# Performance work log

Hardware: AMD Instinct MI355X
Metric: run time of the kernel (lower is better)

Reference implementation:

```python
import jax, jax.numpy as jnp
from jax import lax
import numpy as np

KSIZE = 21

def setup_inputs() -> dict:
    key = jax.random.key(0)
    k1, k2 = jax.random.split(key)
    x = jax.random.normal(k1, (32, 3, 512, 512), dtype=jnp.float32)
    kernel = jax.random.uniform(k2, (32, 1, KSIZE, KSIZE), dtype=jnp.float32)
    return {"x": x, "kernel": kernel}

def reference(x, kernel):
    # Per-sample depthwise conv: fuse batch loop into a single grouped conv
    # by folding batch into channels (groups = B*C).
    B, C, H, W = x.shape
    K = kernel.shape[-1]
    pad = K // 2
    # expand the per-sample kernel across channels, shape (B*C, 1, K, K)
    k = jnp.broadcast_to(kernel, (B, C, K, K)).reshape(B * C, 1, K, K)
    xr = x.reshape(1, B * C, H, W)
    out = lax.conv_general_dilated(
        xr, k,
        window_strides=(1, 1),
        padding=[(pad, pad), (pad, pad)],
        dimension_numbers=("NCHW", "OIHW", "NCHW"),
        feature_group_count=B * C,
    )
    return out.reshape(B, C, H, W)
```

## Files before the change

### kernel.cpp

```cpp
#include <hip/hip_runtime.h>

#define KK 21
#define HH 512
#define WW 512
#define CC 3
#define BB 32
#define TILE_Y 64
#define TILE_X 128
#define SROWS 84
#define SSTRIDE 168
#define NB_PER_B 21504
#define NCHUNK 41

typedef __attribute__((ext_vector_type(8))) short short8;
typedef __attribute__((ext_vector_type(4))) float floatx4;

__device__ __forceinline__ unsigned short f2bf(float f) {
    union { float f; unsigned u; } v; v.f = f;
    unsigned r = v.u + 0x7FFF + ((v.u >> 16) & 1);
    return (unsigned short)(r >> 16);
}

__global__ __launch_bounds__(256) void build_B(
    const float* __restrict__ ker, unsigned short* __restrict__ wsB)
{
    const int b = blockIdx.x;
    const float* __restrict__ kp = ker + b * KK * KK;
    unsigned short* __restrict__ wb = wsB + (size_t)b * NB_PER_B;
    for (int e = threadIdx.x; e < NB_PER_B; e += 256) {
        const int j  = e & 7;
        const int n  = (e >> 3) & 15;
        const int q  = (e >> 7) & 3;
        const int h  = (e >> 9) & 1;
        const int kh = e >> 10;
        const int d  = q * 8 + j - n;
        float v = 0.0f;
        if (h == 0) { if (d >= 0 && d < 16) v = kp[kh * KK + d]; }
        else        { if (d >= 0 && d < 5)  v = kp[kh * KK + 16 + d]; }
        wb[e] = f2bf(v);
    }
}

__global__ __launch_bounds__(256, 5) void dwconv_mfma(
    const float* __restrict__ x,
    const unsigned short* __restrict__ wsB,
    float* __restrict__ out)
{
    __shared__ __align__(16) unsigned short s_in[SROWS * SSTRIDE];

    const int tiles = (HH / TILE_Y) * (WW / TILE_X);
    const int bc = blockIdx.x / tiles;
    const int t  = blockIdx.x % tiles;
    const int ty0 = (t / (WW / TILE_X)) * TILE_Y;
    const int tx0 = (t % (WW / TILE_X)) * TILE_X;
    const int b = bc / CC;

    const float* __restrict__ xp = x + (size_t)bc * HH * WW;
    const unsigned short* __restrict__ wsb = wsB + (size_t)b * NB_PER_B;
    const int tid = threadIdx.x;

    for (int i = tid; i < SROWS * NCHUNK; i += 256) {
        const int ly = i / NCHUNK;
        const int k  = i - ly * NCHUNK;
        const int gy = ty0 - 10 + ly;
        const int gx0 = tx0 - 12 + 4 * k;
        const int lc0 = 4 * k - 2;
        float4 v = make_float4(0.f, 0.f, 0.f, 0.f);
        if (gy >= 0 && gy < HH) {
            const float* __restrict__ rp = xp + (size_t)gy * WW;
            if (gx0 >= 0 && gx0 + 3 < WW) {
                v = *(const float4*)(rp + gx0);
            } else {
                if (gx0 + 0 >= 0 && gx0 + 0 < WW) v.x = rp[gx0 + 0];
                if (gx0 + 1 >= 0 && gx0 + 1 < WW) v.y = rp[gx0 + 1];
                if (gx0 + 2 >= 0 && gx0 + 2 < WW) v.z = rp[gx0 + 2];
                if (gx0 + 3 >= 0 && gx0 + 3 < WW) v.w = rp[gx0 + 3];
            }
        }
        const unsigned p0 = (unsigned)f2bf(v.x) | ((unsigned)f2bf(v.y) << 16);
        const unsigned p1 = (unsigned)f2bf(v.z) | ((unsigned)f2bf(v.w) << 16);
        unsigned* row = (unsigned*)&s_in[ly * SSTRIDE];
        if (lc0 >= 0) row[lc0 >> 1] = p0;
        row[(lc0 >> 1) + 1] = p1;
    }
    __syncthreads();

    const int lane = tid & 63;
    const int wv   = tid >> 6;
    const int mrow = lane & 15;
    const int qd   = lane >> 4;

    floatx4 acc[8];
#pragma unroll
    for (int tt = 0; tt < 8; ++tt) acc[tt] = (floatx4){0.f, 0.f, 0.f, 0.f};

    const unsigned short* bbase = wsb + (qd * 16 + mrow) * 8;
    short8 nb1 = *(const short8*)(bbase);
    short8 nb2 = *(const short8*)(bbase + 512);

#pragma unroll 1
    for (int kh = 0; kh < KK; ++kh) {
        const short8 b1 = nb1;
        const short8 b2 = nb2;
        const int khn = (kh < KK - 1) ? (kh + 1) : kh;
        nb1 = *(const short8*)(bbase + khn * 1024);
        nb2 = *(const short8*)(bbase + khn * 1024 + 512);

        const unsigned short* arow = s_in + (16 * wv + kh + mrow) * SSTRIDE + 8 * qd;
        short8 a[9];
#pragma unroll
        for (int s = 0; s < 9; ++s) a[s] = *(const short8*)(arow + 16 * s);

#pragma unroll
        for (int tt = 0; tt < 8; ++tt) {
            acc[tt] = __builtin_amdgcn_mfma_f32_16x16x32_bf16(a[tt],     b1, acc[tt], 0, 0, 0);
            acc[tt] = __builtin_amdgcn_mfma_f32_16x16x32_bf16(a[tt + 1], b2, acc[tt], 0, 0, 0);
        }
    }

    float* __restrict__ op = out + (size_t)bc * HH * WW;
#pragma unroll
    for (int tt = 0; tt < 8; ++tt) {
#pragma unroll
        for (int r = 0; r < 4; ++r) {
            const int y = ty0 + 16 * wv + qd * 4 + r;
            const int xcol = tx0 + 16 * tt + mrow;
            op[(size_t)y * WW + xcol] = acc[tt][r];
        }
    }
}

extern "C" void kernel_launch(void* const* d_in, const int* in_sizes, int n_in,
                              void* d_out, int out_size, void* d_ws, size_t ws_size,
                              hipStream_t stream) {
    const float* x   = (const float*)d_in[0];
    const float* ker = (const float*)d_in[1];
    float* out = (float*)d_out;
    unsigned short* wsB = (unsigned short*)d_ws;

    build_B<<<BB, 256, 0, stream>>>(ker, wsB);

    const int tiles = (HH / TILE_Y) * (WW / TILE_X);
    const int nblocks = BB * CC * tiles;
    dwconv_mfma<<<nblocks, 256, 0, stream>>>(x, wsB, out);
}
```

Measured before the change: 243.3 us.

## Pack two kernel rows per MFMA K-dimension to cut wasted MFMA work

Repacks the banded bf16 weight matrix so each 32-wide MFMA K slice covers two filter rows, and iterates over 11 row pairs with three MFMAs per output tile instead of 21 rows with two. This reduces the number of MFMA instructions and LDS A-fragment loads spent on zero padding. The input staging loop now loads 8 floats per thread and writes one 16-byte LDS store. Launch bounds are lowered to 4 waves per SIMD, which lowers occupancy in exchange for more registers.

```diff
diff --git a/kernel.cpp b/kernel.cpp
--- a/kernel.cpp
+++ b/kernel.cpp
@@ -7,10 +7,11 @@
 #define BB 32
 #define TILE_Y 64
 #define TILE_X 128
-#define SROWS 84
+#define SROWS 85
 #define SSTRIDE 168
-#define NB_PER_B 21504
-#define NCHUNK 41
+#define NKHP 11
+#define NB_PER_B (NKHP * 3 * 512)
+#define NCHUNK 20
 
 typedef __attribute__((ext_vector_type(8))) short short8;
 typedef __attribute__((ext_vector_type(4))) float floatx4;
@@ -28,20 +29,24 @@
     const float* __restrict__ kp = ker + b * KK * KK;
     unsigned short* __restrict__ wb = wsB + (size_t)b * NB_PER_B;
     for (int e = threadIdx.x; e < NB_PER_B; e += 256) {
-        const int j  = e & 7;
-        const int n  = (e >> 3) & 15;
-        const int q  = (e >> 7) & 3;
-        const int h  = (e >> 9) & 1;
-        const int kh = e >> 10;
-        const int d  = q * 8 + j - n;
+        const int j    = e & 7;
+        const int n    = (e >> 3) & 15;
+        const int q    = (e >> 7) & 3;
+        const int f    = e >> 9;
+        const int khp  = f / 3;
+        const int half = f - khp * 3;
+        const int k    = q * 8 + j;
+        const int h    = k >> 4;
+        const int c    = k & 15;
+        const int kh   = 2 * khp + h;
+        const int d    = c - n - 2 + 16 * half;
         float v = 0.0f;
-        if (h == 0) { if (d >= 0 && d < 16) v = kp[kh * KK + d]; }
-        else        { if (d >= 0 && d < 5)  v = kp[kh * KK + 16 + d]; }
+        if (kh < KK && d >= 0 && d < KK) v = kp[kh * KK + d];
         wb[e] = f2bf(v);
     }
 }
 
-__global__ __launch_bounds__(256, 5) void dwconv_mfma(
+__global__ __launch_bounds__(256, 4) void dwconv_mfma(
     const float* __restrict__ x,
     const unsigned short* __restrict__ wsB,
     float* __restrict__ out)
@@ -60,28 +65,33 @@
     const int tid = threadIdx.x;
 
     for (int i = tid; i < SROWS * NCHUNK; i += 256) {
-        const int ly = i / NCHUNK;
-        const int k  = i - ly * NCHUNK;
-        const int gy = ty0 - 10 + ly;
-        const int gx0 = tx0 - 12 + 4 * k;
-        const int lc0 = 4 * k - 2;
-        float4 v = make_float4(0.f, 0.f, 0.f, 0.f);
+        const int ly  = i / NCHUNK;
+        const int k   = i - ly * NCHUNK;
+        const int gy  = ty0 - 10 + ly;
+        const int gx0 = tx0 - 12 + 8 * k;
+        float4 v0 = make_float4(0.f, 0.f, 0.f, 0.f);
+        float4 v1 = make_float4(0.f, 0.f, 0.f, 0.f);
         if (gy >= 0 && gy < HH) {
             const float* __restrict__ rp = xp + (size_t)gy * WW;
-            if (gx0 >= 0 && gx0 + 3 < WW) {
-                v = *(const float4*)(rp + gx0);
+            if (gx0 >= 0 && gx0 + 7 < WW) {
+                v0 = *(const float4*)(rp + gx0);
+                v1 = *(const float4*)(rp + gx0 + 4);
             } else {
-                if (gx0 + 0 >= 0 && gx0 + 0 < WW) v.x = rp[gx0 + 0];
-                if (gx0 + 1 >= 0 && gx0 + 1 < WW) v.y = rp[gx0 + 1];
-                if (gx0 + 2 >= 0 && gx0 + 2 < WW) v.z = rp[gx0 + 2];
-                if (gx0 + 3 >= 0 && gx0 + 3 < WW) v.w = rp[gx0 + 3];
+                if (gx0 + 0 >= 0 && gx0 + 0 < WW) v0.x = rp[gx0 + 0];
+                if (gx0 + 1 >= 0 && gx0 + 1 < WW) v0.y = rp[gx0 + 1];
+                if (gx0 + 2 >= 0 && gx0 + 2 < WW) v0.z = rp[gx0 + 2];
+                if (gx0 + 3 >= 0 && gx0 + 3 < WW) v0.w = rp[gx0 + 3];
+                if (gx0 + 4 >= 0 && gx0 + 4 < WW) v1.x = rp[gx0 + 4];
+                if (gx0 + 5 >= 0 && gx0 + 5 < WW) v1.y = rp[gx0 + 5];
+                if (gx0 + 6 >= 0 && gx0 + 6 < WW) v1.z = rp[gx0 + 6];
+                if (gx0 + 7 >= 0 && gx0 + 7 < WW) v1.w = rp[gx0 + 7];
             }
         }
-        const unsigned p0 = (unsigned)f2bf(v.x) | ((unsigned)f2bf(v.y) << 16);
-        const unsigned p1 = (unsigned)f2bf(v.z) | ((unsigned)f2bf(v.w) << 16);
-        unsigned* row = (unsigned*)&s_in[ly * SSTRIDE];
-        if (lc0 >= 0) row[lc0 >> 1] = p0;
-        row[(lc0 >> 1) + 1] = p1;
+        const int p0 = (int)((unsigned)f2bf(v0.x) | ((unsigned)f2bf(v0.y) << 16));
+        const int p1 = (int)((unsigned)f2bf(v0.z) | ((unsigned)f2bf(v0.w) << 16));
+        const int p2 = (int)((unsigned)f2bf(v1.x) | ((unsigned)f2bf(v1.y) << 16));
+        const int p3 = (int)((unsigned)f2bf(v1.z) | ((unsigned)f2bf(v1.w) << 16));
+        *(int4*)&s_in[ly * SSTRIDE + 8 * k] = make_int4(p0, p1, p2, p3);
     }
     __syncthreads();
 
@@ -94,27 +104,33 @@
 #pragma unroll
     for (int tt = 0; tt < 8; ++tt) acc[tt] = (floatx4){0.f, 0.f, 0.f, 0.f};
 
-    const unsigned short* bbase = wsb + (qd * 16 + mrow) * 8;
+    const unsigned short* bbase = wsb + lane * 8;
+    const unsigned short* abase = s_in + ((16 * wv + mrow + (qd >> 1)) * SSTRIDE) + 8 * (qd & 1);
+
     short8 nb1 = *(const short8*)(bbase);
     short8 nb2 = *(const short8*)(bbase + 512);
+    short8 nb3 = *(const short8*)(bbase + 1024);
 
 #pragma unroll 1
-    for (int kh = 0; kh < KK; ++kh) {
+    for (int khp = 0; khp < NKHP; ++khp) {
         const short8 b1 = nb1;
         const short8 b2 = nb2;
-        const int khn = (kh < KK - 1) ? (kh + 1) : kh;
-        nb1 = *(const short8*)(bbase + khn * 1024);
-        nb2 = *(const short8*)(bbase + khn * 1024 + 512);
+        const short8 b3 = nb3;
+        const int khn = (khp < NKHP - 1) ? (khp + 1) : khp;
+        nb1 = *(const short8*)(bbase + khn * 1536);
+        nb2 = *(const short8*)(bbase + khn * 1536 + 512);
+        nb3 = *(const short8*)(bbase + khn * 1536 + 1024);
 
-        const unsigned short* arow = s_in + (16 * wv + kh + mrow) * SSTRIDE + 8 * qd;
-        short8 a[9];
+        const unsigned short* arow = abase + 2 * khp * SSTRIDE;
+        short8 a[10];
 #pragma unroll
-        for (int s = 0; s < 9; ++s) a[s] = *(const short8*)(arow + 16 * s);
+        for (int s = 0; s < 10; ++s) a[s] = *(const short8*)(arow + 16 * s);
 
 #pragma unroll
         for (int tt = 0; tt < 8; ++tt) {
             acc[tt] = __builtin_amdgcn_mfma_f32_16x16x32_bf16(a[tt],     b1, acc[tt], 0, 0, 0);
             acc[tt] = __builtin_amdgcn_mfma_f32_16x16x32_bf16(a[tt + 1], b2, acc[tt], 0, 0, 0);
+            acc[tt] = __builtin_amdgcn_mfma_f32_16x16x32_bf16(a[tt + 2], b3, acc[tt], 0, 0, 0);
         }
     }
 
```

Measured after the change: 217.9 us. -10.4%, faster.
